# Performance work log

Measured on AMD Instinct MI355X. Metric: run time of the kernel, lower is better.

## Reference

```python
import jax, jax.numpy as jnp
import numpy as np

B, H, W, C = 32, 56, 56, 384
HEADS, WIN, SHIFT = 12, 7, 3
MLP_HID = 4 * C
N = WIN * WIN
EPS = 1e-5


def _rel_pos_index(win):
    ch, cw = np.meshgrid(np.arange(win), np.arange(win), indexing='ij')
    coords = np.stack([ch.ravel(), cw.ravel()])            # (2, N)
    rel = coords[:, :, None] - coords[:, None, :]          # (2, N, N)
    rel = rel.transpose(1, 2, 0).astype(np.int64)
    rel[:, :, 0] += win - 1
    rel[:, :, 1] += win - 1
    rel[:, :, 0] *= 2 * win - 1
    return rel.sum(-1)                                     # (N, N)


def _attn_mask(Hh, Ww, win, shift):
    img = np.zeros((Hh, Ww))
    cnt = 0
    slices = (slice(0, -win), slice(-win, -shift), slice(-shift, None))
    for hs in slices:
        for ws in slices:
            img[hs, ws] = cnt
            cnt += 1
    m = img.reshape(Hh // win, win, Ww // win, win).transpose(0, 2, 1, 3).reshape(-1, win * win)
    am = m[:, None, :] - m[:, :, None]
    return np.where(am != 0, -100.0, 0.0).astype(np.float32)  # (nW, N, N)


REL_IDX = jnp.asarray(_rel_pos_index(WIN))
ATTN_MASK = jnp.asarray(_attn_mask(H, W, WIN, SHIFT))


def setup_inputs() -> dict:
    key = jax.random.key(0)
    ks = jax.random.split(key, 16)
    s = 0.02
    return {
        'x': jax.random.normal(ks[0], (B, H * W, C), jnp.float32),
        'g1': jnp.ones((C,), jnp.float32),
        'b1': jnp.zeros((C,), jnp.float32),
        'qkv_w': jax.random.normal(ks[1], (3 * C, C), jnp.float32) * s,
        'qkv_b': jnp.zeros((3 * C,), jnp.float32),
        'rel_bias': jax.random.normal(ks[2], ((2 * WIN - 1) ** 2, HEADS), jnp.float32) * s,
        'proj_w': jax.random.normal(ks[3], (C, C), jnp.float32) * s,
        'proj_b': jnp.zeros((C,), jnp.float32),
        'g2': jnp.ones((C,), jnp.float32),
        'b2': jnp.zeros((C,), jnp.float32),
        'fc1_w': jax.random.normal(ks[4], (MLP_HID, C), jnp.float32) * s,
        'fc1_b': jnp.zeros((MLP_HID,), jnp.float32),
        'fc2_w': jax.random.normal(ks[5], (C, MLP_HID), jnp.float32) * s,
        'fc2_b': jnp.zeros((C,), jnp.float32),
    }


def _ln(x, g, b):
    m = x.mean(-1, keepdims=True)
    v = jnp.var(x, axis=-1, keepdims=True)
    return (x - m) * jax.lax.rsqrt(v + EPS) * g + b


def reference(x, g1, b1, qkv_w, qkv_b, rel_bias, proj_w, proj_b, g2, b2, fc1_w, fc1_b, fc2_w, fc2_b):
    Bz, L, Cc = x.shape
    hd = Cc // HEADS
    nWh = H // WIN
    shortcut = x

    h = _ln(x, g1, b1).reshape(Bz, H, W, Cc)
    h = jnp.roll(h, (-SHIFT, -SHIFT), axis=(1, 2))
    # window partition -> (Bz*nW, N, C)
    h = h.reshape(Bz, nWh, WIN, nWh, WIN, Cc).transpose(0, 1, 3, 2, 4, 5).reshape(-1, N, Cc)

    qkv = (h @ qkv_w.T + qkv_b).reshape(-1, N, 3, HEADS, hd).transpose(2, 0, 3, 1, 4)
    q, k, v = qkv[0] * (hd ** -0.5), qkv[1], qkv[2]
    attn = jnp.einsum('bhnd,bhmd->bhnm', q, k)  # (Bz*nW, heads, N, N)

    bias = rel_bias[REL_IDX.reshape(-1)].reshape(N, N, HEADS).transpose(2, 0, 1)
    attn = attn + bias[None]

    nW = ATTN_MASK.shape[0]
    attn = attn.reshape(Bz, nW, HEADS, N, N) + ATTN_MASK[None, :, None]
    attn = jax.nn.softmax(attn, axis=-1).reshape(-1, HEADS, N, N)

    out = jnp.einsum('bhnm,bhmd->bhnd', attn, v).transpose(0, 2, 1, 3).reshape(-1, N, Cc)
    out = out @ proj_w.T + proj_b
    # window reverse + unshift
    out = out.reshape(Bz, nWh, nWh, WIN, WIN, Cc).transpose(0, 1, 3, 2, 4, 5).reshape(Bz, H, W, Cc)
    out = jnp.roll(out, (SHIFT, SHIFT), axis=(1, 2)).reshape(Bz, L, Cc)

    x = shortcut + out
    h2 = _ln(x, g2, b2)
    h2 = jax.nn.gelu(h2 @ fc1_w.T + fc1_b, approximate=False)
    h2 = h2 @ fc2_w.T + fc2_b
    return x + h2
```

## Files before the change

kernel.cpp:

```cpp
#include <hip/hip_runtime.h>
#include <hip/hip_bf16.h>
#include <math.h>

#define B_      32
#define H_      56
#define W_      56
#define C_      384
#define HEADS_  12
#define WIN_    7
#define SHIFT_  3
#define NTOK_   49
#define HD_     32
#define T_      100352
#define MLP_    1536
#define TCH_    50176

typedef __bf16 bf16x8 __attribute__((ext_vector_type(8)));
typedef unsigned short u16x8 __attribute__((ext_vector_type(8)));
typedef float  f32x4  __attribute__((ext_vector_type(4)));

__device__ __forceinline__ float bf2f(unsigned short u) {
  union { unsigned int i; float f; } v; v.i = ((unsigned int)u) << 16; return v.f;
}
__device__ __forceinline__ unsigned short f2bf(float f) {
  union { float f; unsigned int i; } v; v.f = f;
  unsigned int x = v.i;
  return (unsigned short)((x + 0x7fffu + ((x >> 16) & 1u)) >> 16);
}
__device__ __forceinline__ float gelu_fast(float x) {
  const float t = 0.79788456f * x * (1.0f + 0.044715f * x * x);
  const float e = __expf(2.0f * t);
  const float th = 1.0f - 2.0f / (e + 1.0f);
  return 0.5f * x * (1.0f + th);
}
__device__ __forceinline__ void gload_lds16(const void* g, void* l) {
  __builtin_amdgcn_global_load_lds(
      (const __attribute__((address_space(1))) void*)g,
      (__attribute__((address_space(3))) void*)l, 16, 0, 0);
}
__device__ __forceinline__ bf16x8 ldg8(const unsigned short* p) {
  u16x8 v = *(const u16x8*)p;
  return __builtin_bit_cast(bf16x8, v);
}

__global__ __launch_bounds__(256)
void prologue_kernel(const float* __restrict__ s0, unsigned short* __restrict__ d0,
                     const float* __restrict__ s1, unsigned short* __restrict__ d1,
                     const float* __restrict__ s2, unsigned short* __restrict__ d2,
                     const float* __restrict__ s3, unsigned short* __restrict__ d3,
                     const float* __restrict__ rel_bias, float* __restrict__ biasx,
                     const float* __restrict__ x, const float* __restrict__ g1,
                     const float* __restrict__ b1, unsigned short* __restrict__ xw) {
  int b = blockIdx.x;
  if (b < 1728) {
    const float* src; unsigned short* dst;
    if (b < 432)       { src = s0; dst = d0; }
    else if (b < 576)  { src = s1; dst = d1; b -= 432; }
    else if (b < 1152) { src = s2; dst = d2; b -= 576; }
    else               { src = s3; dst = d3; b -= 1152; }
    const int i = (b * 256 + threadIdx.x) * 4;
    const float4 v = *(const float4*)(src + i);
    ushort4 o;
    o.x = f2bf(v.x); o.y = f2bf(v.y); o.z = f2bf(v.z); o.w = f2bf(v.w);
    *(ushort4*)(dst + i) = o;
    return;
  }
  if (b < 1875) {
    const int hi = (b - 1728) * 4 + (threadIdx.x >> 6);
    const int j = threadIdx.x & 63;
    if (hi < HEADS_ * NTOK_) {
      const int head = hi / NTOK_, i = hi - head * NTOK_;
      float v = 0.f;
      if (j < NTOK_) {
        const int ih = i / 7, iw = i - ih * 7;
        const int jh = j / 7, jw = j - jh * 7;
        const int ridx = (ih - jh + 6) * 13 + (iw - jw + 6);
        v = rel_bias[ridx * HEADS_ + head];
      }
      biasx[(size_t)hi * 64 + j] = v;
    }
    return;
  }
  {
    const int m = (b - 1875) * 4 + (threadIdx.x >> 6);
    const int lane = threadIdx.x & 63;
    int w = m / NTOK_, t = m - w * NTOK_;
    int bz = w >> 6, widx = w & 63;
    int wh = widx >> 3, ww = widx & 7;
    int ih = t / WIN_, iw = t - ih * WIN_;
    int gh = (wh * WIN_ + ih + SHIFT_) % H_;
    int gw = (ww * WIN_ + iw + SHIFT_) % W_;
    const size_t srcoff = ((size_t)bz * (H_ * W_) + gh * W_ + gw) * C_;
    const float2* row2 = (const float2*)(x + srcoff);
    float2 v[3]; float sa = 0.f, sb = 0.f;
#pragma unroll
    for (int u = 0; u < 3; ++u) {
      v[u] = row2[lane + 64 * u];
      sa += v[u].x + v[u].y;
      sb += v[u].x * v[u].x + v[u].y * v[u].y;
    }
#pragma unroll
    for (int off = 32; off; off >>= 1) {
      sa += __shfl_xor(sa, off);
      sb += __shfl_xor(sb, off);
    }
    const float mean = sa * (1.0f / C_);
    const float var  = sb * (1.0f / C_) - mean * mean;
    const float rstd = rsqrtf(var + 1e-5f);
    unsigned short* orow = xw + (size_t)m * C_;
#pragma unroll
    for (int u = 0; u < 3; ++u) {
      const int cc = (lane + 64 * u) * 2;
      ushort2 o;
      o.x = f2bf((v[u].x - mean) * rstd * g1[cc]     + b1[cc]);
      o.y = f2bf((v[u].y - mean) * rstd * g1[cc + 1] + b1[cc + 1]);
      *(ushort2*)(orow + cc) = o;
    }
  }
}

__global__ __launch_bounds__(256)
void ln_kernel(const float* __restrict__ xin, const float* __restrict__ g,
               const float* __restrict__ bb, unsigned short* __restrict__ outbf) {
  const int m = blockIdx.x * 4 + (threadIdx.x >> 6);
  const int lane = threadIdx.x & 63;
  const float2* row2 = (const float2*)(xin + (size_t)m * C_);
  float2 v[3]; float s = 0.f, s2 = 0.f;
#pragma unroll
  for (int u = 0; u < 3; ++u) {
    v[u] = row2[lane + 64 * u];
    s  += v[u].x + v[u].y;
    s2 += v[u].x * v[u].x + v[u].y * v[u].y;
  }
#pragma unroll
  for (int off = 32; off; off >>= 1) {
    s  += __shfl_xor(s, off);
    s2 += __shfl_xor(s2, off);
  }
  const float mean = s * (1.0f / C_);
  const float var  = s2 * (1.0f / C_) - mean * mean;
  const float rstd = rsqrtf(var + 1e-5f);
  unsigned short* orow = outbf + (size_t)m * C_;
#pragma unroll
  for (int u = 0; u < 3; ++u) {
    const int c = (lane + 64 * u) * 2;
    ushort2 o;
    o.x = f2bf((v[u].x - mean) * rstd * g[c]     + bb[c]);
    o.y = f2bf((v[u].y - mean) * rstd * g[c + 1] + bb[c + 1]);
    *(ushort2*)(orow + c) = o;
  }
}

#define BM 256
#define BN 128
#define BKg 64

template<int EPI>
__global__ __launch_bounds__(512)
void mfma_gemm(const unsigned short* __restrict__ A,
               const unsigned short* __restrict__ Wb,
               const float* __restrict__ bias,
               void* __restrict__ outv,
               const float* __restrict__ resid,
               int M, int Nn, int K) {
  __shared__ unsigned short Al[BM * BKg];
  __shared__ unsigned short Bl[BN * BKg];
  const int t    = threadIdx.x;
  const int wid  = t >> 6;
  const int lane = t & 63;
  const int wr   = wid >> 1, wc = wid & 1;

  const unsigned int nb = gridDim.x * gridDim.y;
  const unsigned int lin = blockIdx.y * gridDim.x + blockIdx.x;
  const unsigned int q = nb >> 3, r = nb & 7;
  const unsigned int xcd = lin & 7, idx = lin >> 3;
  const unsigned int wg = (xcd < r ? xcd * (q + 1) : r * (q + 1) + (xcd - r) * q) + idx;
  const int m0 = (int)(wg / gridDim.x) * BM;
  const int n0 = (int)(wg % gridDim.x) * BN;

  f32x4 acc[4][4] = {};

  const int sr8    = lane >> 3;
  const int schunk = (lane & 7) ^ (sr8 & 7);
  const int fr  = lane & 15;
  const int fq  = lane >> 4;

  for (int k0 = 0; k0 < K; k0 += BKg) {
    __syncthreads();
#pragma unroll
    for (int i = 0; i < 4; ++i) {
      const int rr = i * 64 + wid * 8 + sr8;
      gload_lds16(A + (size_t)(m0 + rr) * K + k0 + schunk * 8,
                  (void*)(Al + (size_t)(i * 64 + wid * 8) * BKg));
    }
#pragma unroll
    for (int i = 0; i < 2; ++i) {
      const int rr = i * 64 + wid * 8 + sr8;
      gload_lds16(Wb + (size_t)(n0 + rr) * K + k0 + schunk * 8,
                  (void*)(Bl + (size_t)(i * 64 + wid * 8) * BKg));
    }
    __syncthreads();

#pragma unroll
    for (int kk = 0; kk < 2; ++kk) {
      bf16x8 af[4], bfr[4];
#pragma unroll
      for (int mi = 0; mi < 4; ++mi) {
        const int row = wr * 64 + mi * 16 + fr;
        const int ch  = (kk * 4 + fq) ^ (row & 7);
        af[mi] = *(const bf16x8*)(Al + (size_t)row * BKg + ch * 8);
      }
#pragma unroll
      for (int ni = 0; ni < 4; ++ni) {
        const int row = wc * 64 + ni * 16 + fr;
        const int ch  = (kk * 4 + fq) ^ (row & 7);
        bfr[ni] = *(const bf16x8*)(Bl + (size_t)row * BKg + ch * 8);
      }
#pragma unroll
      for (int mi = 0; mi < 4; ++mi)
#pragma unroll
        for (int ni = 0; ni < 4; ++ni)
          acc[mi][ni] = __builtin_amdgcn_mfma_f32_16x16x32_bf16(
              af[mi], bfr[ni], acc[mi][ni], 0, 0, 0);
    }
  }

  const int ecol  = fr;
  const int erow0 = fq * 4;
#pragma unroll
  for (int mi = 0; mi < 4; ++mi) {
#pragma unroll
    for (int r2 = 0; r2 < 4; ++r2) {
      const int m = m0 + wr * 64 + mi * 16 + erow0 + r2;
      size_t dstbase = 0;
      if (EPI == 2) {
        int w = m / NTOK_, tt = m - w * NTOK_;
        int bz = w >> 6, widx = w & 63;
        int wh = widx >> 3, ww = widx & 7;
        int ih = tt / WIN_, iw = tt - ih * WIN_;
        int gh = (wh * WIN_ + ih + SHIFT_) % H_;
        int gw = (ww * WIN_ + iw + SHIFT_) % W_;
        dstbase = ((size_t)bz * (H_ * W_) + gh * W_ + gw) * C_;
      }
#pragma unroll
      for (int ni = 0; ni < 4; ++ni) {
        const int n = n0 + wc * 64 + ni * 16 + ecol;
        float val = acc[mi][ni][r2] + bias[n];
        if (EPI == 0) {
          ((unsigned short*)outv)[(size_t)m * Nn + n] = f2bf(val);
        } else if (EPI == 1) {
          ((unsigned short*)outv)[(size_t)m * Nn + n] = f2bf(gelu_fast(val));
        } else if (EPI == 2) {
          ((float*)outv)[dstbase + n] = resid[dstbase + n] + val;
        } else {
          float* o = (float*)outv + (size_t)m * Nn + n;
          *o += val;
        }
      }
    }
  }
}

#define AW 2
__global__ __launch_bounds__(64 * AW)
void attn_mfma_kernel(const unsigned short* __restrict__ qkv,
                      const float* __restrict__ biasx,
                      unsigned short* __restrict__ out) {
  __shared__ unsigned short sP[AW][64 * 72];
  __shared__ unsigned short sVT[AW][32 * 72];
  __shared__ float sRI[AW][64];
  const int wid  = threadIdx.x >> 6;
  const int lane = threadIdx.x & 63;
  const int task = blockIdx.x * AW + wid;
  const int w    = task / HEADS_;
  const int head = task - w * HEADS_;
  const int widx = w & 63;
  const int wh = widx >> 3, ww = widx & 7;
  const bool edge = (wh == 7) || (ww == 7);
  const int c  = lane & 15;
  const int fq = lane >> 4;
  unsigned short* Pl = sP[wid];
  unsigned short* Vl = sVT[wid];
  float* Ri = sRI[wid];
  const unsigned short* qw = qkv + (size_t)w * NTOK_ * (3 * C_);

  u16x8 vv[4];
#pragma unroll
  for (int p = 0; p < 4; ++p)
    vv[p] = *(const u16x8*)(qw + (size_t)(p * 16 + c) * (3 * C_) + 2 * C_ + head * HD_ + fq * 8);

  bf16x8 kf[4], qf[4];
#pragma unroll
  for (int nj = 0; nj < 4; ++nj)
    kf[nj] = ldg8(qw + (size_t)(nj * 16 + c) * (3 * C_) + C_ + head * HD_ + fq * 8);
#pragma unroll
  for (int qi = 0; qi < 4; ++qi)
    qf[qi] = ldg8(qw + (size_t)(qi * 16 + c) * (3 * C_) + head * HD_ + fq * 8);

  const f32x4 zero4 = {0.f, 0.f, 0.f, 0.f};
  f32x4 accT[4][4];
  __builtin_amdgcn_s_setprio(1);
#pragma unroll
  for (int nj = 0; nj < 4; ++nj)
#pragma unroll
    for (int qi = 0; qi < 4; ++qi)
      accT[nj][qi] = __builtin_amdgcn_mfma_f32_16x16x32_bf16(kf[nj], qf[qi], zero4, 0, 0, 0);
  __builtin_amdgcn_s_setprio(0);

#pragma unroll
  for (int p = 0; p < 4; ++p)
#pragma unroll
    for (int u = 0; u < 8; ++u) {
      const int d  = fq * 8 + u;
      const int ch = (2 * p + (c >> 3)) ^ ((u + fq) & 7);
      Vl[d * 72 + ch * 8 + (c & 7)] = (unsigned short)vv[p][u];
    }

  int lj16[16];
  unsigned jpad = 0;
#pragma unroll
  for (int tt = 0; tt < 16; ++tt) {
    const int j = (tt >> 2) * 16 + fq * 4 + (tt & 3);
    int lj = 0;
    if (j >= NTOK_) jpad |= (1u << tt);
    else if (edge) {
      const int jh = j / 7, jw2 = j - jh * 7;
      const int shj = wh * 7 + jh, swj = ww * 7 + jw2;
      lj = (shj < 49 ? 0 : (shj < 53 ? 1 : 2)) * 3 + (swj < 49 ? 0 : (swj < 53 ? 1 : 2));
    }
    lj16[tt] = lj;
  }

  const float* bh = biasx + (size_t)head * (NTOK_ * 64);
#pragma unroll
  for (int qi = 0; qi < 4; ++qi) {
    const int i  = qi * 16 + c;
    const int ic = i < NTOK_ ? i : 0;
    int li = 0;
    if (edge) {
      const int ih = ic / 7, iw2 = ic - ih * 7;
      const int shi = wh * 7 + ih, swi = ww * 7 + iw2;
      li = (shi < 49 ? 0 : (shi < 53 ? 1 : 2)) * 3 + (swi < 49 ? 0 : (swi < 53 ? 1 : 2));
    }
    float sv[16];
#pragma unroll
    for (int nj = 0; nj < 4; ++nj) {
      const float4 b4 = *(const float4*)(bh + ic * 64 + nj * 16 + fq * 4);
      const float* b4p = (const float*)&b4;
#pragma unroll
      for (int r = 0; r < 4; ++r) {
        const int tt = nj * 4 + r;
        float s = accT[nj][qi][r] * 0.17677669529663687f + b4p[r];
        if (edge && lj16[tt] != li) s -= 100.f;
        if (jpad & (1u << tt)) s = -1e30f;
        sv[tt] = s;
      }
    }
    float mx = sv[0];
#pragma unroll
    for (int tt = 1; tt < 16; ++tt) mx = fmaxf(mx, sv[tt]);
    mx = fmaxf(mx, __shfl_xor(mx, 16));
    mx = fmaxf(mx, __shfl_xor(mx, 32));
    float e[16]; float sm = 0.f;
#pragma unroll
    for (int tt = 0; tt < 16; ++tt) { e[tt] = __expf(sv[tt] - mx); sm += e[tt]; }
    sm += __shfl_xor(sm, 16);
    sm += __shfl_xor(sm, 32);
    if (fq == 0) Ri[i] = 1.0f / sm;
#pragma unroll
    for (int nj = 0; nj < 4; ++nj) {
      ushort4 pk;
      pk.x = f2bf(e[nj * 4 + 0]); pk.y = f2bf(e[nj * 4 + 1]);
      pk.z = f2bf(e[nj * 4 + 2]); pk.w = f2bf(e[nj * 4 + 3]);
      *(ushort4*)(Pl + (size_t)i * 72 + nj * 16 + fq * 4) = pk;
    }
  }

  f32x4 accO[4][2] = {};
#pragma unroll
  for (int kk = 0; kk < 2; ++kk) {
    bf16x8 ap[4], bv[2];
#pragma unroll
    for (int mi = 0; mi < 4; ++mi)
      ap[mi] = __builtin_bit_cast(bf16x8,
          *(const u16x8*)(Pl + (mi * 16 + c) * 72 + kk * 32 + fq * 8));
#pragma unroll
    for (int nd = 0; nd < 2; ++nd) {
      const int row = nd * 16 + c;
      const int ch  = (kk * 4 + fq) ^ ((row + (row >> 3)) & 7);
      bv[nd] = __builtin_bit_cast(bf16x8, *(const u16x8*)(Vl + row * 72 + ch * 8));
    }
    __builtin_amdgcn_s_setprio(1);
#pragma unroll
    for (int mi = 0; mi < 4; ++mi)
#pragma unroll
      for (int nd = 0; nd < 2; ++nd)
        accO[mi][nd] = __builtin_amdgcn_mfma_f32_16x16x32_bf16(ap[mi], bv[nd], accO[mi][nd], 0, 0, 0);
    __builtin_amdgcn_s_setprio(0);
  }

#pragma unroll
  for (int mi = 0; mi < 4; ++mi)
#pragma unroll
    for (int r = 0; r < 4; ++r) {
      const int i = mi * 16 + fq * 4 + r;
      if (i < NTOK_) {
        const float inv = Ri[i];
#pragma unroll
        for (int nd = 0; nd < 2; ++nd)
          out[(size_t)(w * NTOK_ + i) * C_ + head * HD_ + nd * 16 + c] =
              f2bf(accO[mi][nd][r] * inv);
      }
    }
}

extern "C" void kernel_launch(void* const* d_in, const int* in_sizes, int n_in,
                              void* d_out, int out_size, void* d_ws, size_t ws_size,
                              hipStream_t stream) {
  const float* x        = (const float*)d_in[0];
  const float* g1       = (const float*)d_in[1];
  const float* b1       = (const float*)d_in[2];
  const float* qkv_w    = (const float*)d_in[3];
  const float* qkv_b    = (const float*)d_in[4];
  const float* rel_bias = (const float*)d_in[5];
  const float* proj_w   = (const float*)d_in[6];
  const float* proj_b   = (const float*)d_in[7];
  const float* g2       = (const float*)d_in[8];
  const float* b2       = (const float*)d_in[9];
  const float* fc1_w    = (const float*)d_in[10];
  const float* fc1_b    = (const float*)d_in[11];
  const float* fc2_w    = (const float*)d_in[12];
  const float* fc2_b    = (const float*)d_in[13];
  float* out = (float*)d_out;

  char* ws = (char*)d_ws;
  unsigned short* xw   = (unsigned short*)(ws);
  unsigned short* qkvb = (unsigned short*)(ws + 77070336);
  unsigned short* attn_out = xw;
  unsigned short* h2   = xw;
  unsigned short* hidc = qkvb;
  unsigned short* qkv_wb  = (unsigned short*)(ws + 308412416);
  unsigned short* proj_wb = (unsigned short*)(ws + 309297152);
  unsigned short* fc1_wb  = (unsigned short*)(ws + 309592064);
  unsigned short* fc2_wb  = (unsigned short*)(ws + 310771712);
  float*          biasx   = (float*)(ws + 311951360);

  prologue_kernel<<<dim3(1728 + 147 + T_ / 4), dim3(256), 0, stream>>>(
      qkv_w, qkv_wb, proj_w, proj_wb, fc1_w, fc1_wb, fc2_w, fc2_wb,
      rel_bias, biasx, x, g1, b1, xw);

  mfma_gemm<0><<<dim3(1152 / BN, T_ / BM), dim3(512), 0, stream>>>(
      xw, qkv_wb, qkv_b, (void*)qkvb, nullptr, T_, 1152, 384);

  attn_mfma_kernel<<<dim3((T_ / NTOK_) * HEADS_ / AW), dim3(64 * AW), 0, stream>>>(
      qkvb, biasx, attn_out);

  mfma_gemm<2><<<dim3(384 / BN, T_ / BM), dim3(512), 0, stream>>>(
      attn_out, proj_wb, proj_b, (void*)out, x, T_, 384, 384);

  ln_kernel<<<dim3(T_ / 4), dim3(256), 0, stream>>>(out, g2, b2, h2);

  for (int chk = 0; chk < 2; ++chk) {
    const size_t row0 = (size_t)chk * TCH_;
    mfma_gemm<1><<<dim3(MLP_ / BN, TCH_ / BM), dim3(512), 0, stream>>>(
        h2 + row0 * C_, fc1_wb, fc1_b, (void*)hidc, nullptr, TCH_, MLP_, 384);
    mfma_gemm<3><<<dim3(384 / BN, TCH_ / BM), dim3(512), 0, stream>>>(
        hidc, fc2_wb, fc2_b, (void*)(out + row0 * C_), nullptr, TCH_, 384, MLP_);
  }
}
```

Measured before the change: 883.6 us.

## Double-buffer GEMM LDS tiles with BK=32 and prefetch next k-slice

Reworks the MFMA GEMM main loop into a two-stage software pipeline. The K tile is halved to 32 and two LDS buffers are allocated, so the next slice's global-to-LDS loads are issued before the current slice's MFMAs. This removes one barrier per iteration and is meant to hide load latency behind compute. The swizzle pattern is changed to fit the 4-chunk rows. The trade-off is twice as many loop iterations, with less MFMA work per barrier.

```diff
diff --git a/kernel.cpp b/kernel.cpp
--- a/kernel.cpp
+++ b/kernel.cpp
@@ -153,7 +153,7 @@
 
 #define BM 256
 #define BN 128
-#define BKg 64
+#define BKg 32
 
 template<int EPI>
 __global__ __launch_bounds__(512)
@@ -163,8 +163,8 @@
                void* __restrict__ outv,
                const float* __restrict__ resid,
                int M, int Nn, int K) {
-  __shared__ unsigned short Al[BM * BKg];
-  __shared__ unsigned short Bl[BN * BKg];
+  __shared__ unsigned short Al[2][BM * BKg];
+  __shared__ unsigned short Bl[2][BN * BKg];
   const int t    = threadIdx.x;
   const int wid  = t >> 6;
   const int lane = t & 63;
@@ -180,50 +180,61 @@
 
   f32x4 acc[4][4] = {};
 
-  const int sr8    = lane >> 3;
-  const int schunk = (lane & 7) ^ (sr8 & 7);
   const int fr  = lane & 15;
   const int fq  = lane >> 4;
-
-  for (int k0 = 0; k0 < K; k0 += BKg) {
+  const int nk  = K / BKg;
+
+#define STAGE_(kt, buf)                                                        \
+  {                                                                            \
+    const int kb = (kt) * BKg;                                                 \
+    _Pragma("unroll")                                                          \
+    for (int i = 0; i < 2; ++i) {                                              \
+      const int ix = i * 512 + t;                                              \
+      const int rw = ix >> 2;                                                  \
+      const int sc = (ix & 3) ^ ((ix >> 3) & 3);                               \
+      gload_lds16(A + (size_t)(m0 + rw) * K + kb + sc * 8,                     \
+                  (void*)(&Al[buf][(i * 512 + wid * 64) * 8]));                \
+    }                                                                          \
+    {                                                                          \
+      const int rw = t >> 2;                                                   \
+      const int sc = (t & 3) ^ ((t >> 3) & 3);                                 \
+      gload_lds16(Wb + (size_t)(n0 + rw) * K + kb + sc * 8,                    \
+                  (void*)(&Bl[buf][(wid * 64) * 8]));                          \
+    }                                                                          \
+  }
+
+  STAGE_(0, 0);
+  __syncthreads();
+
+  for (int ks = 0; ks < nk; ++ks) {
+    const int cur = ks & 1;
+    if (ks + 1 < nk) STAGE_(ks + 1, cur ^ 1);
+
+    const unsigned short* Ab = &Al[cur][0];
+    const unsigned short* Bb = &Bl[cur][0];
+    bf16x8 af[4], bfr[4];
+#pragma unroll
+    for (int mi = 0; mi < 4; ++mi) {
+      const int row = wr * 64 + mi * 16 + fr;
+      const int ch  = fq ^ ((row >> 1) & 3);
+      af[mi] = *(const bf16x8*)(Ab + (size_t)row * BKg + ch * 8);
+    }
+#pragma unroll
+    for (int ni = 0; ni < 4; ++ni) {
+      const int row = wc * 64 + ni * 16 + fr;
+      const int ch  = fq ^ ((row >> 1) & 3);
+      bfr[ni] = *(const bf16x8*)(Bb + (size_t)row * BKg + ch * 8);
+    }
+#pragma unroll
+    for (int mi = 0; mi < 4; ++mi)
+#pragma unroll
+      for (int ni = 0; ni < 4; ++ni)
+        acc[mi][ni] = __builtin_amdgcn_mfma_f32_16x16x32_bf16(
+            af[mi], bfr[ni], acc[mi][ni], 0, 0, 0);
+
     __syncthreads();
-#pragma unroll
-    for (int i = 0; i < 4; ++i) {
-      const int rr = i * 64 + wid * 8 + sr8;
-      gload_lds16(A + (size_t)(m0 + rr) * K + k0 + schunk * 8,
-                  (void*)(Al + (size_t)(i * 64 + wid * 8) * BKg));
-    }
-#pragma unroll
-    for (int i = 0; i < 2; ++i) {
-      const int rr = i * 64 + wid * 8 + sr8;
-      gload_lds16(Wb + (size_t)(n0 + rr) * K + k0 + schunk * 8,
-                  (void*)(Bl + (size_t)(i * 64 + wid * 8) * BKg));
-    }
-    __syncthreads();
-
-#pragma unroll
-    for (int kk = 0; kk < 2; ++kk) {
-      bf16x8 af[4], bfr[4];
-#pragma unroll
-      for (int mi = 0; mi < 4; ++mi) {
-        const int row = wr * 64 + mi * 16 + fr;
-        const int ch  = (kk * 4 + fq) ^ (row & 7);
-        af[mi] = *(const bf16x8*)(Al + (size_t)row * BKg + ch * 8);
-      }
-#pragma unroll
-      for (int ni = 0; ni < 4; ++ni) {
-        const int row = wc * 64 + ni * 16 + fr;
-        const int ch  = (kk * 4 + fq) ^ (row & 7);
-        bfr[ni] = *(const bf16x8*)(Bl + (size_t)row * BKg + ch * 8);
-      }
-#pragma unroll
-      for (int mi = 0; mi < 4; ++mi)
-#pragma unroll
-        for (int ni = 0; ni < 4; ++ni)
-          acc[mi][ni] = __builtin_amdgcn_mfma_f32_16x16x32_bf16(
-              af[mi], bfr[ni], acc[mi][ni], 0, 0, 0);
-    }
-  }
+  }
+#undef STAGE_
 
   const int ecol  = fr;
   const int erow0 = fq * 4;
```

Result: slower. 926.4 us (+4.8%).
